# Kernel optimization log

Measured on AMD Instinct MI355X. Metric: run time of the kernel, lower is better.

Reference implementation:

```python
import jax, jax.numpy as jnp
import numpy as np

TWO_PI = 2.0 * np.pi
EPS = 1e-6

# mixture packed layout along last axis (7): [weight, px, py, cxx, cxy, cyx, cyy]

def unpack(m):
    w = m[..., 0]
    p = m[..., 1:3]
    C = m[..., 3:7].reshape(m.shape[:-1] + (2, 2))
    return w, p, C

def pack(w, p, C):
    return jnp.concatenate([w[..., None], p, C.reshape(C.shape[:-2] + (4,))], axis=-1)

def det2(C):
    return C[..., 0, 0] * C[..., 1, 1] - C[..., 0, 1] * C[..., 1, 0]

def inv2(C):
    d = det2(C)[..., None, None]
    adj = jnp.stack([
        jnp.stack([C[..., 1, 1], -C[..., 0, 1]], axis=-1),
        jnp.stack([-C[..., 1, 0], C[..., 0, 0]], axis=-1)], axis=-2)
    return adj / d

def component_integrals(w, C):
    # integral of an amplitude-parameterized 2D gaussian: w * 2*pi * sqrt(det C)
    return w * TWO_PI * jnp.sqrt(jnp.maximum(det2(C), EPS))

def gm_convolve(data, kernel):
    # data [B,Li,Nd,7], kernel [Lo,Li,Nk,7] -> [B,Lo,Li*Nd*Nk,7]
    wd, pd, Cd = unpack(data)
    wk, pk, Ck = unpack(kernel)
    dd = det2(Cd)[:, None, :, :, None]              # [B,1,Li,Nd,1]
    dk = det2(Ck)[None, :, :, None, :]              # [1,Lo,Li,1,Nk]
    Cs = Cd[:, None, :, :, None, :, :] + Ck[None, :, :, None, :, :, :]  # [B,Lo,Li,Nd,Nk,2,2]
    ps = pd[:, None, :, :, None, :] + pk[None, :, :, None, :, :]        # [B,Lo,Li,Nd,Nk,2]
    # amplitude of convolved gaussian so that integrals multiply
    ws = (wd[:, None, :, :, None] * wk[None, :, :, None, :]
          * TWO_PI * jnp.sqrt(dd * dk / jnp.maximum(det2(Cs), EPS)))
    m = pack(ws, ps, Cs)
    B, Lo = m.shape[0], m.shape[1]
    return m.reshape(B, Lo, -1, 7)

def eval_at_centers(w, p, C):
    # value of the whole mixture at each component center; [.., N]
    Ci = inv2(C)                                        # [..,N,2,2]
    diff = p[..., :, None, :] - p[..., None, :, :]      # [..,K,N,2]
    md = jnp.einsum('...kni,...nij,...knj->...kn', diff, Ci, diff)
    return jnp.einsum('...n,...kn->...k', w, jnp.exp(-0.5 * md))

def relu_fit(m, bias, n_out):
    # fitting-based ReLU: rescale each component so the mixture matches
    # relu(m(x)+b) at the centers, then keep the n_out largest components
    w, p, C = unpack(m)
    v = eval_at_centers(w, p, C) + bias[None, :, None]  # [B,L,N]
    scale = jax.nn.relu(v) / (jnp.abs(v) + EPS)
    w2 = w * scale
    _, idx = jax.lax.top_k(jnp.abs(w2), n_out)          # [B,L,n_out]
    w_s = jnp.take_along_axis(w2, idx, axis=-1)
    p_s = jnp.take_along_axis(p, jnp.broadcast_to(idx[..., None], idx.shape + (2,)), axis=-2)
    Cf = C.reshape(C.shape[:-2] + (4,))
    C_s = jnp.take_along_axis(Cf, jnp.broadcast_to(idx[..., None], idx.shape + (4,)), axis=-2)
    return pack(w_s, p_s, C_s.reshape(C_s.shape[:-1] + (2, 2)))

def batchnorm(m, per_gaussian):
    w, p, C = unpack(m)
    tot = jnp.sum(jnp.abs(component_integrals(w, C)), axis=-1, keepdims=True)  # [B,L,1]
    if not per_gaussian:
        tot = jnp.mean(tot, axis=0, keepdims=True)      # batch statistic per channel
    return pack(w / (tot + EPS), p, C)

def integrate(m):
    w, _, C = unpack(m)
    return jnp.sum(component_integrals(w, C), axis=-1)  # [B,L]

def forward(in_x, kernel1, kernel2, kernel3, bias1, bias2, bias3):
    x = batchnorm(in_x, per_gaussian=True)   # bn0
    x = gm_convolve(x, kernel1)              # [B,5,320,7]
    x = relu_fit(x, bias1, 25)
    x = batchnorm(x, per_gaussian=False)
    x = gm_convolve(x, kernel2)              # [B,6,625,7]
    x = relu_fit(x, bias2, 12)
    x = batchnorm(x, per_gaussian=False)
    x = gm_convolve(x, kernel3)              # [B,10,360,7]
    x = relu_fit(x, bias3, 5)
    x = batchnorm(x, per_gaussian=False)
    out = jax.nn.log_softmax(integrate(x), axis=1)
    return out.reshape(-1, 10)

def _make_kernel(key, lo, li, nk, weight_sd, position_range, covariance_range):
    kw, kp = jax.random.split(key)
    w = jax.random.normal(kw, (lo, li, nk)) * weight_sd
    p = jax.random.uniform(kp, (lo, li, nk, 2), minval=-position_range, maxval=position_range)
    C = jnp.broadcast_to(covariance_range * jnp.eye(2), (lo, li, nk, 2, 2))
    return pack(w, p, C).astype(jnp.float32)

def setup_inputs() -> dict:
    key = jax.random.key(0)
    k = jax.random.split(key, 8)
    B, NIN, NK = 32, 64, 5
    w = jax.random.uniform(k[0], (B, 1, NIN), minval=0.05, maxval=1.0)
    p = jax.random.uniform(k[1], (B, 1, NIN, 2), minval=-14.0, maxval=14.0)
    cdiag = jax.random.uniform(k[2], (B, 1, NIN, 2), minval=0.5, maxval=2.0)
    C = jnp.zeros((B, 1, NIN, 2, 2)).at[..., 0, 0].set(cdiag[..., 0]).at[..., 1, 1].set(cdiag[..., 1])
    in_x = pack(w, p, C).astype(jnp.float32)
    return {
        'in_x': in_x,
        'kernel1': _make_kernel(k[3], 5, 1, NK, 0.4, 2.0, 0.5),
        'kernel2': _make_kernel(k[4], 6, 5, NK, 0.04, 4.0, 2.0),
        'kernel3': _make_kernel(k[5], 10, 6, NK, 0.025, 8.0, 4.0),
        'bias1': jnp.zeros((5,), jnp.float32),
        'bias2': jnp.zeros((6,), jnp.float32),
        'bias3': jnp.zeros((10,), jnp.float32),
    }

def reference(in_x, kernel1, kernel2, kernel3, bias1, bias2, bias3):
    return forward(in_x, kernel1, kernel2, kernel3, bias1, bias2, bias3)
```

## Files before the change

kernel.cpp:

```cpp
#include <hip/hip_runtime.h>

#define TWO_PI_F 6.283185307179586f
#define EPS_F 1e-6f
#define LOG2E_F 1.4426950408889634f
#define BATCH 32

#if __has_builtin(__builtin_amdgcn_exp2f)
#define EXP2F(x) __builtin_amdgcn_exp2f(x)
#else
#define EXP2F(x) exp2f(x)
#endif

typedef float v2f __attribute__((ext_vector_type(2)));

__device__ __forceinline__ float sane(float x) {
    return ((__float_as_uint(x) & 0x7f800000u) == 0x7f800000u) ? 0.f : x;
}

template<int LO, int LI, int ND, int NK, int NCOMP, int KOUT,
         int KP, int TPG, int G, bool FIRST>
__global__ __launch_bounds__(TPG*G) void layer_kernel(
    const float* __restrict__ in_x,
    const float* __restrict__ prev_sel,
    const float* __restrict__ prev_tot,
    const float* __restrict__ kern,
    const float* __restrict__ bias,
    float* __restrict__ out_sel,
    float* __restrict__ out_tot)
{
    constexpr int KUSE   = NCOMP / KP;
    static_assert(KUSE * KP == NCOMP, "exact k tiling required");
    constexpr int CHUNK  = (NCOMP + G - 1) / G;
    constexpr int NCOMP4 = (NCOMP + 3) & ~3;
    constexpr int NQn    = NCOMP4 / 4;
    constexpr int CQ     = (NQn + G - 1) / G;
    constexpr int NPAIR  = KP / 2;
    constexpr int PPAD   = NPAIR > 0 ? NPAIR : 1;
    constexpr bool ODD   = (KP & 1) != 0;

    const int b   = blockIdx.x / LO;
    const int lo  = blockIdx.x % LO;
    const int tid = threadIdx.x;
    const int g   = tid / TPG;
    const int kt  = tid % TPG;
    const bool active = (kt < KUSE);

    struct StageT {
        float4 d_c[LI*ND];
        float4 k_c[LI*NK];
        float  d_w[LI*ND], d_px[LI*ND], d_py[LI*ND];
        float  k_w[LI*NK], k_px[LI*NK], k_py[LI*NK];
    };
    constexpr size_t ACCB = (size_t)(G > 1 ? (G-1)*TPG*KP : 1) * sizeof(float);
    constexpr size_t UB   = sizeof(StageT) > ACCB ? sizeof(StageT) : ACCB;
    __shared__ __align__(16) unsigned char u_smem[UB];
    StageT& st    = *reinterpret_cast<StageT*>(u_smem);
    float* accbuf = reinterpret_cast<float*>(u_smem);

    __shared__ float2 cPos[NCOMP];
    __shared__ float4 nP[NCOMP];
    __shared__ float4 nQ[NCOMP];
    __shared__ float4 cC[NCOMP];
    __shared__ float  w2s[NCOMP];
    __shared__ __align__(16) float a2s[NCOMP4];
    __shared__ float  scr[64];
    __shared__ float  selint[32];
    __shared__ float  dscale[LI];

    if constexpr (FIRST) {
        if (tid < ND) {
            const float* s = in_x + (size_t)(b*ND + tid)*7;
            const float w  = sane(s[0]);
            const float c0 = sane(s[3]), c1 = sane(s[4]), c2 = sane(s[5]), c3 = sane(s[6]);
            st.d_w[tid] = w; st.d_px[tid] = sane(s[1]); st.d_py[tid] = sane(s[2]);
            st.d_c[tid] = make_float4(c0, c1, c2, c3);
            const float det = c0*c3 - c1*c2;
            scr[tid] = sane(fabsf(w) * TWO_PI_F * sqrtf(fmaxf(det, EPS_F)));
        }
        __syncthreads();
        if (tid == 0) {
            float s = 0.f;
            for (int i = 0; i < ND; ++i) s += scr[i];
            dscale[0] = 1.f / (s + EPS_F);
        }
        __syncthreads();
        if (tid < ND) st.d_w[tid] = sane(st.d_w[tid] * dscale[0]);
    } else {
        if (tid < LI) {
            float s = 0.f;
            for (int bb = 0; bb < BATCH; ++bb) s += prev_tot[bb*LI + tid];
            dscale[tid] = 1.f / (s / (float)BATCH + EPS_F);
        }
        __syncthreads();
        if (tid < LI*ND) {
            const int li = tid / ND;
            const float* s = prev_sel + (size_t)(b*LI*ND + tid)*7;
            st.d_w[tid]  = sane(s[0] * dscale[li]);
            st.d_px[tid] = s[1]; st.d_py[tid] = s[2];
            st.d_c[tid]  = make_float4(s[3], s[4], s[5], s[6]);
        }
    }
    if (tid < LI*NK) {
        const float* s = kern + (size_t)(lo*LI*NK + tid)*7;
        st.k_w[tid]  = sane(s[0]);
        st.k_px[tid] = sane(s[1]); st.k_py[tid] = sane(s[2]);
        st.k_c[tid]  = make_float4(sane(s[3]), sane(s[4]), sane(s[5]), sane(s[6]));
    }
    __syncthreads();

    if (tid < NCOMP) {
        const int li = tid / (ND*NK);
        const int r  = tid % (ND*NK);
        const int nd = r / NK, nk = r % NK;
        const int di = li*ND + nd, ki = li*NK + nk;
        const float4 dc = st.d_c[di], kc = st.k_c[ki];
        const float c0 = dc.x + kc.x, c1 = dc.y + kc.y, c2 = dc.z + kc.z, c3 = dc.w + kc.w;
        const float dd = dc.x*dc.w - dc.y*dc.z;
        const float dk = kc.x*kc.w - kc.y*kc.z;
        const float ds = c0*c3 - c1*c2;
        const float w  = sane(st.d_w[di]*st.k_w[ki]*TWO_PI_F*sqrtf(fmaxf(dd*dk, 0.f) / fmaxf(ds, EPS_F)));
        const float px = sane(st.d_px[di] + st.k_px[ki]);
        const float py = sane(st.d_py[di] + st.k_py[ki]);
        const float inv = -0.5f * LOG2E_F / ds;
        const float a   = sane(c3*inv);
        const float bb  = sane(-(c1 + c2)*inv);
        const float cc  = sane(c0*inv);
        const float dd2 = sane(-(2.f*a*px + bb*py));
        const float ee  = sane(-(2.f*cc*py + bb*px));
        const float ff  = sane((a*px + bb*py)*px + cc*py*py);
        cPos[tid] = make_float2(px, py);
        nP[tid]   = make_float4(a, bb, cc, dd2);
        nQ[tid]   = make_float4(ee, ff, w, 0.f);
        cC[tid]   = make_float4(sane(c0), sane(c1), sane(c2), sane(c3));
    }
    __syncthreads();

    v2f kxP[PPAD], kyP[PPAD], kx2P[PPAD], ky2P[PPAD], kxyP[PPAD], accP[PPAD];
    float kxS = 0.f, kyS = 0.f, kx2S = 0.f, ky2S = 0.f, kxyS = 0.f, accS = 0.f;
    #pragma unroll
    for (int p = 0; p < NPAIR; ++p) {
        float x0 = 0.f, y0 = 0.f, x1 = 0.f, y1 = 0.f;
        if (active) {
            const float2 p0 = cPos[kt + (2*p    )*KUSE];
            const float2 p1 = cPos[kt + (2*p + 1)*KUSE];
            x0 = p0.x; y0 = p0.y; x1 = p1.x; y1 = p1.y;
        }
        v2f kx; kx.x = x0; kx.y = x1;
        v2f ky; ky.x = y0; ky.y = y1;
        kxP[p] = kx; kyP[p] = ky;
        kx2P[p] = kx*kx; ky2P[p] = ky*ky; kxyP[p] = kx*ky;
        v2f z; z.x = 0.f; z.y = 0.f; accP[p] = z;
    }
    if constexpr (ODD) {
        if (active) { const float2 pz = cPos[kt + (KP-1)*KUSE]; kxS = pz.x; kyS = pz.y; }
        kx2S = kxS*kxS; ky2S = kyS*kyS; kxyS = kxS*kyS;
    }
    {
        const int n0 = g*CHUNK;
        const int n1 = (n0 + CHUNK < NCOMP) ? (n0 + CHUNK) : NCOMP;
        if (n0 < n1) {
            float4 P = nP[n0], Q = nQ[n0];
            #pragma unroll 2
            for (int n = n0; n < n1; ++n) {
                const int nn = (n + 1 < n1) ? n + 1 : n0;
                const float4 Pn = nP[nn];
                const float4 Qn = nQ[nn];
                v2f Pa; Pa.x = P.x; Pa.y = P.x;
                v2f Pb; Pb.x = P.y; Pb.y = P.y;
                v2f Pc; Pc.x = P.z; Pc.y = P.z;
                v2f Pd; Pd.x = P.w; Pd.y = P.w;
                v2f Qe; Qe.x = Q.x; Qe.y = Q.x;
                v2f Qf; Qf.x = Q.y; Qf.y = Q.y;
                v2f Qw; Qw.x = Q.z; Qw.y = Q.z;
                #pragma unroll
                for (int p = 0; p < NPAIR; ++p) {
                    const v2f md = __builtin_elementwise_fma(Pa, kx2P[p],
                                   __builtin_elementwise_fma(Pb, kxyP[p],
                                   __builtin_elementwise_fma(Pc, ky2P[p],
                                   __builtin_elementwise_fma(Pd, kxP[p],
                                   __builtin_elementwise_fma(Qe, kyP[p], Qf)))));
                    v2f ex; ex.x = EXP2F(md.x); ex.y = EXP2F(md.y);
                    accP[p] = __builtin_elementwise_fma(Qw, ex, accP[p]);
                }
                if constexpr (ODD) {
                    const float md = fmaf(P.x, kx2S,
                                     fmaf(P.y, kxyS,
                                     fmaf(P.z, ky2S,
                                     fmaf(P.w, kxS,
                                     fmaf(Q.x, kyS, Q.y)))));
                    accS = fmaf(Q.z, EXP2F(md), accS);
                }
                P = Pn; Q = Qn;
            }
        }
    }
    float acc[KP];
    #pragma unroll
    for (int p = 0; p < NPAIR; ++p) { acc[2*p] = accP[p].x; acc[2*p+1] = accP[p].y; }
    if constexpr (ODD) acc[KP-1] = accS;

    if (g > 0 && active) {
        #pragma unroll
        for (int j = 0; j < KP; ++j) accbuf[((g-1)*TPG + kt)*KP + j] = acc[j];
    }
    __syncthreads();

    const float bi = bias[lo];
    if (g == 0 && active) {
        #pragma unroll
        for (int j = 0; j < KP; ++j) {
            float s = acc[j];
            for (int gg = 1; gg < G; ++gg) s += accbuf[((gg-1)*TPG + kt)*KP + j];
            const float v  = s + bi;
            const float sc = fmaxf(v, 0.f) / (fabsf(v) + EPS_F);
            const int   k  = kt + j*KUSE;
            const float ww = sane(nQ[k].z * sc);
            w2s[k] = ww;
            a2s[k] = fabsf(ww);
        }
    }
    if constexpr (NCOMP4 > NCOMP) {
        if (tid >= NCOMP && tid < NCOMP4) a2s[tid] = -1.f;
    }
    __syncthreads();

    int rank[KP];
    float myv[KP];
    #pragma unroll
    for (int j = 0; j < KP; ++j) rank[j] = 0;
    if (active) {
        #pragma unroll
        for (int j = 0; j < KP; ++j) myv[j] = a2s[kt + j*KUSE];
        const int q0 = g*CQ;
        const int q1 = (q0 + CQ < NQn) ? (q0 + CQ) : NQn;
        for (int q = q0; q < q1; ++q) {
            const float4 v4 = ((const float4*)a2s)[q];
            #pragma unroll
            for (int c = 0; c < 4; ++c) {
                const float vj = (c == 0) ? v4.x : (c == 1) ? v4.y : (c == 2) ? v4.z : v4.w;
                const int   jj = 4*q + c;
                #pragma unroll
                for (int j = 0; j < KP; ++j) {
                    const int myk = kt + j*KUSE;
                    rank[j] += (vj > myv[j] || (vj == myv[j] && jj < myk)) ? 1 : 0;
                }
            }
        }
        if (g > 0) {
            #pragma unroll
            for (int j = 0; j < KP; ++j) accbuf[((g-1)*TPG + kt)*KP + j] = (float)rank[j];
        }
    }
    __syncthreads();

    if (g == 0 && active) {
        #pragma unroll
        for (int j = 0; j < KP; ++j) {
            int r = rank[j];
            for (int gg = 1; gg < G; ++gg) r += (int)accbuf[((gg-1)*TPG + kt)*KP + j];
            if (r < KOUT) {
                const int k = kt + j*KUSE;
                const float2 p = cPos[k];
                const float4 c = cC[k];
                const float ww = w2s[k];
                float* dst = out_sel + (size_t)((b*LO + lo)*KOUT + r)*7;
                dst[0] = ww; dst[1] = p.x; dst[2] = p.y;
                dst[3] = c.x; dst[4] = c.y; dst[5] = c.z; dst[6] = c.w;
                const float det = c.x*c.w - c.y*c.z;
                selint[r] = sane(fabsf(ww) * TWO_PI_F * sqrtf(fmaxf(det, EPS_F)));
            }
        }
    }
    __syncthreads();
    if (tid == 0) {
        float s = 0.f;
        for (int i = 0; i < KOUT; ++i) s += selint[i];
        out_tot[b*LO + lo] = s;
    }
}

__global__ __launch_bounds__(64) void final_kernel(
    const float* __restrict__ sel3,
    const float* __restrict__ tot3,
    float* __restrict__ out)
{
    const int b = blockIdx.x;
    const int tid = threadIdx.x;
    __shared__ float scale3[10], integ[10], red2[2];
    if (tid < 10) {
        float s = 0.f;
        for (int bb = 0; bb < BATCH; ++bb) s += tot3[bb*10 + tid];
        scale3[tid] = 1.f / (s / (float)BATCH + EPS_F);
    }
    __syncthreads();
    if (tid < 10) {
        float s = 0.f;
        const float* base = sel3 + (size_t)((b*10 + tid)*5)*7;
        for (int kk = 0; kk < 5; ++kk) {
            const float* c = base + kk*7;
            const float det = c[3]*c[6] - c[4]*c[5];
            s += c[0] * scale3[tid] * TWO_PI_F * sqrtf(fmaxf(det, EPS_F));
        }
        integ[tid] = sane(s);
    }
    __syncthreads();
    if (tid == 0) {
        float m = -1e30f;
        for (int l = 0; l < 10; ++l) m = fmaxf(m, integ[l]);
        float ss = 0.f;
        for (int l = 0; l < 10; ++l) ss += __expf(integ[l] - m);
        red2[0] = m; red2[1] = logf(ss);
    }
    __syncthreads();
    if (tid < 10) out[b*10 + tid] = integ[tid] - red2[0] - red2[1];
}

extern "C" void kernel_launch(void* const* d_in, const int* in_sizes, int n_in,
                              void* d_out, int out_size, void* d_ws, size_t ws_size,
                              hipStream_t stream)
{
    const float* in_x = (const float*)d_in[0];
    const float* k1   = (const float*)d_in[1];
    const float* k2   = (const float*)d_in[2];
    const float* k3   = (const float*)d_in[3];
    const float* b1   = (const float*)d_in[4];
    const float* b2   = (const float*)d_in[5];
    const float* b3   = (const float*)d_in[6];
    float* out = (float*)d_out;

    float* ws = (float*)d_ws;
    float* sel1 = ws;
    float* tot1 = ws + 28000;
    float* sel2 = ws + 28160;
    float* tot2 = ws + 44288;
    float* sel3 = ws + 44480;
    float* tot3 = ws + 55680;

    layer_kernel<5, 1, 64, 5, 320, 25, 5, 64, 16, true><<<BATCH*5, 1024, 0, stream>>>(
        in_x, nullptr, nullptr, k1, b1, sel1, tot1);
    layer_kernel<6, 5, 25, 5, 625, 12, 5, 128, 8, false><<<BATCH*6, 1024, 0, stream>>>(
        nullptr, sel1, tot1, k2, b2, sel2, tot2);
    layer_kernel<10, 6, 12, 5, 360, 5, 6, 64, 12, false><<<BATCH*10, 768, 0, stream>>>(
        nullptr, sel2, tot2, k3, b3, sel3, tot3);
    final_kernel<<<BATCH, 64, 0, stream>>>(sel3, tot3, out);
}
```

Before: 146.6 us.

## Split each layer block across multiple workgroups with last-block reduction via atomic counter

Each (batch, output-channel) pair is now handled by several smaller workgroups. Each one evaluates a slice of the mixture-at-centers sum and writes its partial sums to global scratch. The last block to finish, found through an atomic counter, reduces the partials, applies the ReLU rescale and runs the top-k ranking, with one thread per component instead of grouped ranks. The aim is to spread work over more CUs than the 160–320 large blocks used before. In exchange it adds global traffic, a memset launch, threadfence overhead, and a serial tail in the last block.

After: 571.0 us. 289% more time.

```diff
diff --git a/kernel.cpp b/kernel.cpp
--- a/kernel.cpp
+++ b/kernel.cpp
@@ -18,45 +18,48 @@
 }
 
 template<int LO, int LI, int ND, int NK, int NCOMP, int KOUT,
-         int KP, int TPG, int G, bool FIRST>
-__global__ __launch_bounds__(TPG*G) void layer_kernel(
+         int KP, int TPG, int G, int NSPLIT, bool FIRST>
+__global__ __launch_bounds__(TPG*(G/NSPLIT)) void layer_kernel(
     const float* __restrict__ in_x,
     const float* __restrict__ prev_sel,
     const float* __restrict__ prev_tot,
     const float* __restrict__ kern,
     const float* __restrict__ bias,
     float* __restrict__ out_sel,
-    float* __restrict__ out_tot)
+    float* __restrict__ out_tot,
+    float* __restrict__ gpart,
+    int*   __restrict__ ctr)
 {
     constexpr int KUSE   = NCOMP / KP;
     static_assert(KUSE * KP == NCOMP, "exact k tiling required");
+    static_assert(G % NSPLIT == 0, "split along group boundaries");
+    constexpr int GBLK   = G / NSPLIT;
+    constexpr int NT     = TPG * GBLK;
     constexpr int CHUNK  = (NCOMP + G - 1) / G;
     constexpr int NCOMP4 = (NCOMP + 3) & ~3;
     constexpr int NQn    = NCOMP4 / 4;
-    constexpr int CQ     = (NQn + G - 1) / G;
     constexpr int NPAIR  = KP / 2;
     constexpr int PPAD   = NPAIR > 0 ? NPAIR : 1;
     constexpr bool ODD   = (KP & 1) != 0;
-
-    const int b   = blockIdx.x / LO;
-    const int lo  = blockIdx.x % LO;
+    static_assert(NT >= LI*ND && NT >= LI*NK && NT >= LI, "one-pass staging");
+    static_assert(!FIRST || NT >= ND, "scr staging");
+
+    const int s   = blockIdx.x % NSPLIT;
+    const int blo = blockIdx.x / NSPLIT;
+    const int lo  = blo % LO;
+    const int b   = blo / LO;
     const int tid = threadIdx.x;
-    const int g   = tid / TPG;
+    const int gl  = tid / TPG;
+    const int gg  = s*GBLK + gl;
     const int kt  = tid % TPG;
     const bool active = (kt < KUSE);
 
-    struct StageT {
+    __shared__ struct {
         float4 d_c[LI*ND];
         float4 k_c[LI*NK];
         float  d_w[LI*ND], d_px[LI*ND], d_py[LI*ND];
         float  k_w[LI*NK], k_px[LI*NK], k_py[LI*NK];
-    };
-    constexpr size_t ACCB = (size_t)(G > 1 ? (G-1)*TPG*KP : 1) * sizeof(float);
-    constexpr size_t UB   = sizeof(StageT) > ACCB ? sizeof(StageT) : ACCB;
-    __shared__ __align__(16) unsigned char u_smem[UB];
-    StageT& st    = *reinterpret_cast<StageT*>(u_smem);
-    float* accbuf = reinterpret_cast<float*>(u_smem);
-
+    } st;
     __shared__ float2 cPos[NCOMP];
     __shared__ float4 nP[NCOMP];
     __shared__ float4 nQ[NCOMP];
@@ -66,52 +69,53 @@
     __shared__ float  scr[64];
     __shared__ float  selint[32];
     __shared__ float  dscale[LI];
+    __shared__ int    sLast;
 
     if constexpr (FIRST) {
         if (tid < ND) {
-            const float* s = in_x + (size_t)(b*ND + tid)*7;
-            const float w  = sane(s[0]);
-            const float c0 = sane(s[3]), c1 = sane(s[4]), c2 = sane(s[5]), c3 = sane(s[6]);
-            st.d_w[tid] = w; st.d_px[tid] = sane(s[1]); st.d_py[tid] = sane(s[2]);
+            const float* sp = in_x + (size_t)(b*ND + tid)*7;
+            const float w  = sane(sp[0]);
+            const float c0 = sane(sp[3]), c1 = sane(sp[4]), c2 = sane(sp[5]), c3 = sane(sp[6]);
+            st.d_w[tid] = w; st.d_px[tid] = sane(sp[1]); st.d_py[tid] = sane(sp[2]);
             st.d_c[tid] = make_float4(c0, c1, c2, c3);
             const float det = c0*c3 - c1*c2;
             scr[tid] = sane(fabsf(w) * TWO_PI_F * sqrtf(fmaxf(det, EPS_F)));
         }
         __syncthreads();
         if (tid == 0) {
-            float s = 0.f;
-            for (int i = 0; i < ND; ++i) s += scr[i];
-            dscale[0] = 1.f / (s + EPS_F);
+            float ssum = 0.f;
+            for (int i = 0; i < ND; ++i) ssum += scr[i];
+            dscale[0] = 1.f / (ssum + EPS_F);
         }
         __syncthreads();
         if (tid < ND) st.d_w[tid] = sane(st.d_w[tid] * dscale[0]);
     } else {
         if (tid < LI) {
-            float s = 0.f;
-            for (int bb = 0; bb < BATCH; ++bb) s += prev_tot[bb*LI + tid];
-            dscale[tid] = 1.f / (s / (float)BATCH + EPS_F);
+            float ssum = 0.f;
+            for (int bb = 0; bb < BATCH; ++bb) ssum += prev_tot[bb*LI + tid];
+            dscale[tid] = 1.f / (ssum / (float)BATCH + EPS_F);
         }
         __syncthreads();
         if (tid < LI*ND) {
             const int li = tid / ND;
-            const float* s = prev_sel + (size_t)(b*LI*ND + tid)*7;
-            st.d_w[tid]  = sane(s[0] * dscale[li]);
-            st.d_px[tid] = s[1]; st.d_py[tid] = s[2];
-            st.d_c[tid]  = make_float4(s[3], s[4], s[5], s[6]);
+            const float* sp = prev_sel + (size_t)(b*LI*ND + tid)*7;
+            st.d_w[tid]  = sane(sp[0] * dscale[li]);
+            st.d_px[tid] = sp[1]; st.d_py[tid] = sp[2];
+            st.d_c[tid]  = make_float4(sp[3], sp[4], sp[5], sp[6]);
         }
     }
     if (tid < LI*NK) {
-        const float* s = kern + (size_t)(lo*LI*NK + tid)*7;
-        st.k_w[tid]  = sane(s[0]);
-        st.k_px[tid] = sane(s[1]); st.k_py[tid] = sane(s[2]);
-        st.k_c[tid]  = make_float4(sane(s[3]), sane(s[4]), sane(s[5]), sane(s[6]));
-    }
-    __syncthreads();
-
-    if (tid < NCOMP) {
-        const int li = tid / (ND*NK);
-        const int r  = tid % (ND*NK);
-        const int nd = r / NK, nk = r % NK;
+        const float* sp = kern + (size_t)(lo*LI*NK + tid)*7;
+        st.k_w[tid]  = sane(sp[0]);
+        st.k_px[tid] = sane(sp[1]); st.k_py[tid] = sane(sp[2]);
+        st.k_c[tid]  = make_float4(sane(sp[3]), sane(sp[4]), sane(sp[5]), sane(sp[6]));
+    }
+    __syncthreads();
+
+    for (int i = tid; i < NCOMP; i += NT) {
+        const int li = i / (ND*NK);
+        const int rr = i % (ND*NK);
+        const int nd = rr / NK, nk = rr % NK;
         const int di = li*ND + nd, ki = li*NK + nk;
         const float4 dc = st.d_c[di], kc = st.k_c[ki];
         const float c0 = dc.x + kc.x, c1 = dc.y + kc.y, c2 = dc.z + kc.z, c3 = dc.w + kc.w;
@@ -128,10 +132,10 @@
         const float dd2 = sane(-(2.f*a*px + bb*py));
         const float ee  = sane(-(2.f*cc*py + bb*px));
         const float ff  = sane((a*px + bb*py)*px + cc*py*py);
-        cPos[tid] = make_float2(px, py);
-        nP[tid]   = make_float4(a, bb, cc, dd2);
-        nQ[tid]   = make_float4(ee, ff, w, 0.f);
-        cC[tid]   = make_float4(sane(c0), sane(c1), sane(c2), sane(c3));
+        cPos[i] = make_float2(px, py);
+        nP[i]   = make_float4(a, bb, cc, dd2);
+        nQ[i]   = make_float4(ee, ff, w, 0.f);
+        cC[i]   = make_float4(sane(c0), sane(c1), sane(c2), sane(c3));
     }
     __syncthreads();
 
@@ -156,7 +160,7 @@
         kx2S = kxS*kxS; ky2S = kyS*kyS; kxyS = kxS*kyS;
     }
     {
-        const int n0 = g*CHUNK;
+        const int n0 = gg*CHUNK;
         const int n1 = (n0 + CHUNK < NCOMP) ? (n0 + CHUNK) : NCOMP;
         if (n0 < n1) {
             float4 P = nP[n0], Q = nQ[n0];
@@ -199,83 +203,63 @@
     for (int p = 0; p < NPAIR; ++p) { acc[2*p] = accP[p].x; acc[2*p+1] = accP[p].y; }
     if constexpr (ODD) acc[KP-1] = accS;
 
-    if (g > 0 && active) {
+    {
+        float* gp = gpart + ((size_t)blo * G + gg) * NCOMP;
+        if (active) {
+            #pragma unroll
+            for (int j = 0; j < KP; ++j) gp[kt + j*KUSE] = acc[j];
+        }
+    }
+
+    __threadfence();
+    __syncthreads();
+    if (tid == 0) sLast = (atomicAdd(ctr + blo, 1) == NSPLIT - 1);
+    __syncthreads();
+    if (!sLast) return;
+    __threadfence();
+
+    const float bi = bias[lo];
+    const float* gbase = gpart + (size_t)blo * G * NCOMP;
+    for (int k = tid; k < NCOMP; k += NT) {
+        float ssum = gbase[k];
         #pragma unroll
-        for (int j = 0; j < KP; ++j) accbuf[((g-1)*TPG + kt)*KP + j] = acc[j];
-    }
-    __syncthreads();
-
-    const float bi = bias[lo];
-    if (g == 0 && active) {
-        #pragma unroll
-        for (int j = 0; j < KP; ++j) {
-            float s = acc[j];
-            for (int gg = 1; gg < G; ++gg) s += accbuf[((gg-1)*TPG + kt)*KP + j];
-            const float v  = s + bi;
-            const float sc = fmaxf(v, 0.f) / (fabsf(v) + EPS_F);
-            const int   k  = kt + j*KUSE;
-            const float ww = sane(nQ[k].z * sc);
-            w2s[k] = ww;
-            a2s[k] = fabsf(ww);
-        }
-    }
-    if constexpr (NCOMP4 > NCOMP) {
-        if (tid >= NCOMP && tid < NCOMP4) a2s[tid] = -1.f;
-    }
-    __syncthreads();
-
-    int rank[KP];
-    float myv[KP];
-    #pragma unroll
-    for (int j = 0; j < KP; ++j) rank[j] = 0;
-    if (active) {
-        #pragma unroll
-        for (int j = 0; j < KP; ++j) myv[j] = a2s[kt + j*KUSE];
-        const int q0 = g*CQ;
-        const int q1 = (q0 + CQ < NQn) ? (q0 + CQ) : NQn;
-        for (int q = q0; q < q1; ++q) {
+        for (int g2 = 1; g2 < G; ++g2) ssum += gbase[(size_t)g2*NCOMP + k];
+        const float v  = ssum + bi;
+        const float sc = fmaxf(v, 0.f) / (fabsf(v) + EPS_F);
+        const float ww = sane(nQ[k].z * sc);
+        w2s[k] = ww;
+        a2s[k] = fabsf(ww);
+    }
+    for (int i = NCOMP + tid; i < NCOMP4; i += NT) a2s[i] = -1.f;
+    __syncthreads();
+
+    for (int k = tid; k < NCOMP; k += NT) {
+        const float mv = a2s[k];
+        int r = 0;
+        for (int q = 0; q < NQn; ++q) {
             const float4 v4 = ((const float4*)a2s)[q];
-            #pragma unroll
-            for (int c = 0; c < 4; ++c) {
-                const float vj = (c == 0) ? v4.x : (c == 1) ? v4.y : (c == 2) ? v4.z : v4.w;
-                const int   jj = 4*q + c;
-                #pragma unroll
-                for (int j = 0; j < KP; ++j) {
-                    const int myk = kt + j*KUSE;
-                    rank[j] += (vj > myv[j] || (vj == myv[j] && jj < myk)) ? 1 : 0;
-                }
-            }
-        }
-        if (g > 0) {
-            #pragma unroll
-            for (int j = 0; j < KP; ++j) accbuf[((g-1)*TPG + kt)*KP + j] = (float)rank[j];
-        }
-    }
-    __syncthreads();
-
-    if (g == 0 && active) {
-        #pragma unroll
-        for (int j = 0; j < KP; ++j) {
-            int r = rank[j];
-            for (int gg = 1; gg < G; ++gg) r += (int)accbuf[((gg-1)*TPG + kt)*KP + j];
-            if (r < KOUT) {
-                const int k = kt + j*KUSE;
-                const float2 p = cPos[k];
-                const float4 c = cC[k];
-                const float ww = w2s[k];
-                float* dst = out_sel + (size_t)((b*LO + lo)*KOUT + r)*7;
-                dst[0] = ww; dst[1] = p.x; dst[2] = p.y;
-                dst[3] = c.x; dst[4] = c.y; dst[5] = c.z; dst[6] = c.w;
-                const float det = c.x*c.w - c.y*c.z;
-                selint[r] = sane(fabsf(ww) * TWO_PI_F * sqrtf(fmaxf(det, EPS_F)));
-            }
+            const int j4 = 4*q;
+            r += (v4.x > mv || (v4.x == mv && j4     < k)) ? 1 : 0;
+            r += (v4.y > mv || (v4.y == mv && j4 + 1 < k)) ? 1 : 0;
+            r += (v4.z > mv || (v4.z == mv && j4 + 2 < k)) ? 1 : 0;
+            r += (v4.w > mv || (v4.w == mv && j4 + 3 < k)) ? 1 : 0;
+        }
+        if (r < KOUT) {
+            const float2 p = cPos[k];
+            const float4 c = cC[k];
+            const float ww = w2s[k];
+            float* dst = out_sel + (size_t)(blo*KOUT + r)*7;
+            dst[0] = ww; dst[1] = p.x; dst[2] = p.y;
+            dst[3] = c.x; dst[4] = c.y; dst[5] = c.z; dst[6] = c.w;
+            const float det = c.x*c.w - c.y*c.z;
+            selint[r] = sane(fabsf(ww) * TWO_PI_F * sqrtf(fmaxf(det, EPS_F)));
         }
     }
     __syncthreads();
     if (tid == 0) {
-        float s = 0.f;
-        for (int i = 0; i < KOUT; ++i) s += selint[i];
-        out_tot[b*LO + lo] = s;
+        float ssum = 0.f;
+        for (int i = 0; i < KOUT; ++i) ssum += selint[i];
+        out_tot[blo] = ssum;
     }
 }
 
@@ -335,12 +319,19 @@
     float* tot2 = ws + 44288;
     float* sel3 = ws + 44480;
     float* tot3 = ws + 55680;
-
-    layer_kernel<5, 1, 64, 5, 320, 25, 5, 64, 16, true><<<BATCH*5, 1024, 0, stream>>>(
-        in_x, nullptr, nullptr, k1, b1, sel1, tot1);
-    layer_kernel<6, 5, 25, 5, 625, 12, 5, 128, 8, false><<<BATCH*6, 1024, 0, stream>>>(
-        nullptr, sel1, tot1, k2, b2, sel2, tot2);
-    layer_kernel<10, 6, 12, 5, 360, 5, 6, 64, 12, false><<<BATCH*10, 768, 0, stream>>>(
-        nullptr, sel2, tot2, k3, b3, sel3, tot3);
+    int*   ctr  = (int*)(ws + 56000);
+    float* gpart = ws + 56672;
+
+    hipMemsetAsync(ctr, 0, 672*sizeof(int), stream);
+
+    layer_kernel<5, 1, 64, 5, 320, 25, 5, 64, 16, 8, true>
+        <<<BATCH*5*8, 128, 0, stream>>>(in_x, nullptr, nullptr, k1, b1,
+                                        sel1, tot1, gpart, ctr);
+    layer_kernel<6, 5, 25, 5, 625, 12, 5, 128, 8, 4, false>
+        <<<BATCH*6*4, 256, 0, stream>>>(nullptr, sel1, tot1, k2, b2,
+                                        sel2, tot2, gpart, ctr + 160);
+    layer_kernel<10, 6, 12, 5, 360, 5, 6, 64, 12, 4, false>
+        <<<BATCH*10*4, 192, 0, stream>>>(nullptr, sel2, tot2, k3, b3,
+                                         sel3, tot3, gpart, ctr + 352);
     final_kernel<<<BATCH, 64, 0, stream>>>(sel3, tot3, out);
 }
```
